# Optimization experiments

Measured on AMD Instinct MI355X. Metric: run time of the kernel, lower is better.

The kernel has to match this reference:

```python
import jax, jax.numpy as jnp
import numpy as np

VOCAB = 10000
EMB = 512
D_IMG = 2048
RNN = 1024
SEQ_LEN = 16
START_TOKEN = VOCAB + 1  # 10001
V_OUT = VOCAB + 3        # 10003


def setup_inputs() -> dict:
    key = jax.random.key(0)
    ks = jax.random.split(key, 24)
    g = lambda k, shape, fan_in: jax.random.normal(k, shape, jnp.float32) / np.sqrt(fan_in)
    inp = {
        "img_features": jax.random.normal(ks[0], (64, 196, D_IMG), jnp.float32),
        "captions": jax.random.randint(ks[1], (64, SEQ_LEN), 0, VOCAB),
        # embedding table
        "emb": g(ks[2], (V_OUT, EMB), EMB),
        # LSTMCell (PyTorch gate order i,f,g,o), stored as [in, 4H]
        "Wih": g(ks[3], (EMB + D_IMG, 4 * RNN), EMB + D_IMG),
        "Whh": g(ks[4], (RNN, 4 * RNN), RNN),
        "bih": jnp.zeros((4 * RNN,), jnp.float32),
        "bhh": jnp.zeros((4 * RNN,), jnp.float32),
        # init_h / init_c
        "Wh0": g(ks[5], (D_IMG, RNN), D_IMG), "bh0": jnp.zeros((RNN,), jnp.float32),
        "Wc0": g(ks[6], (D_IMG, RNN), D_IMG), "bc0": jnp.zeros((RNN,), jnp.float32),
        # f_beta gate
        "Wfb": g(ks[7], (RNN, D_IMG), RNN), "bfb": jnp.zeros((D_IMG,), jnp.float32),
        # deep_output
        "Wout": g(ks[8], (RNN, V_OUT), RNN), "bout": jnp.zeros((V_OUT,), jnp.float32),
        # attention: U (rnn->rnn), W (img->rnn), v (rnn->1)
        "WU": g(ks[9], (RNN, RNN), RNN), "bU": jnp.zeros((RNN,), jnp.float32),
        "WW": g(ks[10], (D_IMG, RNN), D_IMG), "bW": jnp.zeros((RNN,), jnp.float32),
        "Wv": g(ks[11], (RNN, 1), RNN), "bv": jnp.zeros((1,), jnp.float32),
    }
    return inp


def reference(img_features, captions, emb, Wih, Whh, bih, bhh, Wh0, bh0, Wc0, bc0,
              Wfb, bfb, Wout, bout, WU, bU, WW, bW, Wv, bv):
    B = img_features.shape[0]
    # get_target: prepend START token -> [B, T+1]
    start = jnp.full((B, 1), START_TOKEN, dtype=captions.dtype)
    target = jnp.concatenate([start, captions], axis=1)
    embedding = emb[target]                      # [B, T+1, EMB]
    emb_seq = jnp.transpose(embedding, (1, 0, 2))  # [T+1, B, EMB]

    # init LSTM state from mean image features
    avg = img_features.mean(axis=1)              # [B, D_IMG]
    h0 = jnp.tanh(avg @ Wh0 + bh0)
    c0 = jnp.tanh(avg @ Wc0 + bc0)

    # image-side attention projection is timestep-independent
    W_s = img_features @ WW + bW                 # [B, L, RNN]
    b_gates = bih + bhh

    def step(carry, emb_t):
        h, c = carry
        # additive attention
        U_h = h @ WU + bU                        # [B, RNN]
        att = jnp.tanh(W_s + U_h[:, None, :])    # [B, L, RNN]
        e = (att @ Wv).squeeze(-1) + bv          # [B, L]
        alpha = jax.nn.softmax(e, axis=1)
        context = jnp.einsum('bld,bl->bd', img_features, alpha)  # [B, D_IMG]
        gate = jax.nn.sigmoid(h @ Wfb + bfb)
        x = jnp.concatenate([emb_t, gate * context], axis=1)     # [B, EMB+D_IMG]
        # LSTMCell, PyTorch gate order i,f,g,o
        gates = x @ Wih + h @ Whh + b_gates      # [B, 4*RNN]
        i, f, gg, o = jnp.split(gates, 4, axis=1)
        c_new = jax.nn.sigmoid(f) * c + jax.nn.sigmoid(i) * jnp.tanh(gg)
        h_new = jax.nn.sigmoid(o) * jnp.tanh(c_new)
        out = h_new @ Wout + bout                # [B, V_OUT] (dropout=identity, eval mode)
        return (h_new, c_new), (out, alpha)

    (_, _), (preds_t, alphas_t) = jax.lax.scan(step, (h0, c0), emb_seq)
    preds = jnp.transpose(preds_t, (1, 0, 2))    # [B, T+1, V_OUT]
    alphas = jnp.transpose(alphas_t, (1, 0, 2))  # [B, T+1, L]
    return preds, alphas
```

## Files before the change

kernel.cpp:

```cpp
#include <hip/hip_runtime.h>
#include <cstdint>

#define NB    64
#define LIMG  196
#define DIMG  2048
#define RNND  1024
#define EMBD  512
#define TSTEPS 17
#define VOUTD 10003

typedef short bf16x8 __attribute__((ext_vector_type(8)));
typedef float f32x4  __attribute__((ext_vector_type(4)));

__device__ __forceinline__ float fast_sig(float x) {
    return 1.f / (1.f + __expf(-x));
}
__device__ __forceinline__ float fast_tanh(float x) {
    float ax = fabsf(x);
    float e  = __expf(2.f * ax);
    float r  = 1.f - 2.f / (e + 1.f);
    return copysignf(r, x);
}
__device__ __forceinline__ void split_bf(float x, short& hi, short& lo) {
    unsigned u  = __float_as_uint(x);
    unsigned hb = u & 0xffff0000u;
    hi = (short)(u >> 16);
    float r = x - __uint_as_float(hb);
    lo = (short)(__float_as_uint(r) >> 16);
}

__global__ __launch_bounds__(256) void tsplit(
    const float* __restrict__ S1, int ld1,
    const float* __restrict__ S2, int ld2,
    short* __restrict__ outh, short* __restrict__ outl,
    int N, int K, int ksplit, int nsplit)
{
    __shared__ float T[64][65];
    const int k0 = blockIdx.x * 64, n0 = blockIdx.y * 64;
    const int tid = threadIdx.x;
    const int rr = tid >> 2;
    const int cc = (tid & 3) * 16;
    const int kk = k0 + rr;
    const int nn = n0 + cc;
    const float* rp; int col;
    if (nsplit > 0) {
        if (nn >= nsplit) { rp = S2 + (size_t)kk * ld2; col = nn - nsplit; }
        else              { rp = S1 + (size_t)kk * ld1; col = nn; }
    } else {
        if (kk < ksplit)  { rp = S1 + (size_t)kk * ld1; col = nn; }
        else              { rp = S2 + (size_t)(kk - ksplit) * ld2; col = nn; }
    }
#pragma unroll
    for (int j = 0; j < 16; j++)
        T[rr][cc + j] = (nn + j < N) ? rp[col + j] : 0.f;
    __syncthreads();
    const int wn = tid >> 2;
    const int wk = (tid & 3) * 16;
    const int gn = n0 + wn;
    if (gn >= N) return;
    bf16x8 h0, h1, l0, l1;
#pragma unroll
    for (int j = 0; j < 8; j++) {
        short hh, ll;
        split_bf(T[wk + j][wn], hh, ll);     h0[j] = hh; l0[j] = ll;
        split_bf(T[wk + 8 + j][wn], hh, ll); h1[j] = hh; l1[j] = ll;
    }
    const size_t o = (size_t)gn * K + k0 + wk;
    *(bf16x8*)&outh[o]     = h0;
    *(bf16x8*)&outh[o + 8] = h1;
    *(bf16x8*)&outl[o]     = l0;
    *(bf16x8*)&outl[o + 8] = l1;
}

__global__ __launch_bounds__(256) void gemm_bb(
    const float* __restrict__ Af,
    const short* __restrict__ Ah16, const short* __restrict__ Al16,
    const short* __restrict__ Bh16, const short* __restrict__ Bl16,
    const float* __restrict__ bias, float* __restrict__ C,
    int M, int N, int K, int lda, int ldb, int ldc, int pmap,
    int nx, int ny, int gax)
{
    __shared__ short Ah[128 * 40], Al[128 * 40];
    __shared__ short Bh[128 * 40], Bl[128 * 40];

    const int p    = blockIdx.x;
    const int xcd  = p & 7;
    const int slot = p >> 3;
    const int G = gax ? ny : nx;
    const int O = gax ? nx : ny;
    const int qb = G >> 3, qr = G & 7;
    const int cnt = qb + (xcd < qr ? 1 : 0);
    if (slot >= cnt * O) return;
    const int start = xcd * qb + min(xcd, qr);
    const int g = start + slot / O;
    const int o = slot - (slot / O) * O;
    const int n0 = (gax ? o : g) * 128;
    const int m0 = (gax ? g : o) * 128;

    const int tid = threadIdx.x;
    const int lane = tid & 63;
    const int w    = tid >> 6;
    const int wm   = (w >> 1) * 64;
    const int wn   = (w & 1) * 64;
    const int lm   = lane & 15;
    const int lk   = lane >> 4;

    const int ar = tid >> 1;
    const int ac = (tid & 1) * 16;

    f32x4 acc[4][4];
#pragma unroll
    for (int i = 0; i < 4; i++)
#pragma unroll
        for (int j = 0; j < 4; j++) acc[i][j] = (f32x4)0.f;

    for (int k0 = 0; k0 < K; k0 += 32) {
        bf16x8 ah0, ah1, al0, al1;
        if (Af) {
            float f[16];
            if (m0 + ar < M) {
                const float* ap = Af + (size_t)(m0 + ar) * lda + (k0 + ac);
                float4 q0 = *(const float4*)(ap);
                float4 q1 = *(const float4*)(ap + 4);
                float4 q2 = *(const float4*)(ap + 8);
                float4 q3 = *(const float4*)(ap + 12);
                f[0]=q0.x; f[1]=q0.y; f[2]=q0.z; f[3]=q0.w;
                f[4]=q1.x; f[5]=q1.y; f[6]=q1.z; f[7]=q1.w;
                f[8]=q2.x; f[9]=q2.y; f[10]=q2.z; f[11]=q2.w;
                f[12]=q3.x; f[13]=q3.y; f[14]=q3.z; f[15]=q3.w;
            } else {
#pragma unroll
                for (int j = 0; j < 16; j++) f[j] = 0.f;
            }
#pragma unroll
            for (int j = 0; j < 8; j++) {
                short hh, ll;
                split_bf(f[j], hh, ll);     ah0[j] = hh; al0[j] = ll;
                split_bf(f[8 + j], hh, ll); ah1[j] = hh; al1[j] = ll;
            }
        } else {
            const short* pa = Ah16 + (size_t)(m0 + ar) * lda + (k0 + ac);
            ah0 = *(const bf16x8*)pa; ah1 = *(const bf16x8*)(pa + 8);
            const short* qa = Al16 + (size_t)(m0 + ar) * lda + (k0 + ac);
            al0 = *(const bf16x8*)qa; al1 = *(const bf16x8*)(qa + 8);
        }
        const short* pb = Bh16 + (size_t)(n0 + ar) * ldb + (k0 + ac);
        bf16x8 bh0 = *(const bf16x8*)pb, bh1 = *(const bf16x8*)(pb + 8);
        const short* qb2 = Bl16 + (size_t)(n0 + ar) * ldb + (k0 + ac);
        bf16x8 bl0 = *(const bf16x8*)qb2, bl1 = *(const bf16x8*)(qb2 + 8);

        __syncthreads();
        *(bf16x8*)&Ah[ar * 40 + ac]     = ah0;
        *(bf16x8*)&Ah[ar * 40 + ac + 8] = ah1;
        *(bf16x8*)&Al[ar * 40 + ac]     = al0;
        *(bf16x8*)&Al[ar * 40 + ac + 8] = al1;
        *(bf16x8*)&Bh[ar * 40 + ac]     = bh0;
        *(bf16x8*)&Bh[ar * 40 + ac + 8] = bh1;
        *(bf16x8*)&Bl[ar * 40 + ac]     = bl0;
        *(bf16x8*)&Bl[ar * 40 + ac + 8] = bl1;
        __syncthreads();

        bf16x8 afh[4], afl[4], bfh[4], bfl[4];
#pragma unroll
        for (int fm = 0; fm < 4; fm++) {
            const int idx = (wm + fm * 16 + lm) * 40 + lk * 8;
            afh[fm] = *(bf16x8*)&Ah[idx];
            afl[fm] = *(bf16x8*)&Al[idx];
        }
#pragma unroll
        for (int fn = 0; fn < 4; fn++) {
            const int idx = (wn + fn * 16 + lm) * 40 + lk * 8;
            bfh[fn] = *(bf16x8*)&Bh[idx];
            bfl[fn] = *(bf16x8*)&Bl[idx];
        }
#pragma unroll
        for (int fm = 0; fm < 4; fm++)
#pragma unroll
            for (int fn = 0; fn < 4; fn++) {
                acc[fm][fn] = __builtin_amdgcn_mfma_f32_16x16x32_bf16(afh[fm], bfh[fn], acc[fm][fn], 0, 0, 0);
                acc[fm][fn] = __builtin_amdgcn_mfma_f32_16x16x32_bf16(afh[fm], bfl[fn], acc[fm][fn], 0, 0, 0);
                acc[fm][fn] = __builtin_amdgcn_mfma_f32_16x16x32_bf16(afl[fm], bfh[fn], acc[fm][fn], 0, 0, 0);
            }
    }

#pragma unroll
    for (int fm = 0; fm < 4; fm++) {
#pragma unroll
        for (int fn = 0; fn < 4; fn++) {
            const int col = n0 + wn + fn * 16 + lm;
            if (col >= N) continue;
            const float bb = bias ? bias[col] : 0.f;
#pragma unroll
            for (int r = 0; r < 4; r++) {
                const int row = m0 + wm + fm * 16 + lk * 4 + r;
                if (row >= M) continue;
                const size_t orow = pmap ? (size_t)((row & 63) * TSTEPS + (row >> 6))
                                         : (size_t)row;
                C[orow * ldc + col] = acc[fm][fn][r] + bb;
            }
        }
    }
}

__global__ __launch_bounds__(256) void gemm_sk(
    const float* __restrict__ A,
    const short* __restrict__ Bh16, const short* __restrict__ Bl16,
    float* __restrict__ P, int N, int K, int lda, int ldb, int Kc)
{
    __shared__ short Ah[64 * 40], Al[64 * 40];
    __shared__ short Bh[128 * 40], Bl[128 * 40];

    const int tid = threadIdx.x;
    const int n0  = blockIdx.x * 128;
    const int s   = blockIdx.z;
    const int kb  = s * Kc;

    const int lane = tid & 63;
    const int w    = tid >> 6;
    const int wn   = w * 32;
    const int lm   = lane & 15;
    const int lk   = lane >> 4;

    const int a_r = tid >> 2;
    const int a_c = (tid & 3) * 8;
    const int b_r = tid >> 1;
    const int b_c = (tid & 1) * 16;

    f32x4 acc[4][2];
#pragma unroll
    for (int i = 0; i < 4; i++)
#pragma unroll
        for (int j = 0; j < 2; j++) acc[i][j] = (f32x4)0.f;

    for (int k0 = kb; k0 < kb + Kc; k0 += 32) {
        const float* ap = A + (size_t)a_r * lda + (k0 + a_c);
        float4 q0 = *(const float4*)(ap);
        float4 q1 = *(const float4*)(ap + 4);
        float f[8] = {q0.x, q0.y, q0.z, q0.w, q1.x, q1.y, q1.z, q1.w};
        bf16x8 ah, al;
#pragma unroll
        for (int j = 0; j < 8; j++) {
            short hh, ll;
            split_bf(f[j], hh, ll); ah[j] = hh; al[j] = ll;
        }
        const short* pb = Bh16 + (size_t)(n0 + b_r) * ldb + (k0 + b_c);
        bf16x8 bh0 = *(const bf16x8*)pb, bh1 = *(const bf16x8*)(pb + 8);
        const short* qb = Bl16 + (size_t)(n0 + b_r) * ldb + (k0 + b_c);
        bf16x8 bl0 = *(const bf16x8*)qb, bl1 = *(const bf16x8*)(qb + 8);

        __syncthreads();
        *(bf16x8*)&Ah[a_r * 40 + a_c] = ah;
        *(bf16x8*)&Al[a_r * 40 + a_c] = al;
        *(bf16x8*)&Bh[b_r * 40 + b_c]     = bh0;
        *(bf16x8*)&Bh[b_r * 40 + b_c + 8] = bh1;
        *(bf16x8*)&Bl[b_r * 40 + b_c]     = bl0;
        *(bf16x8*)&Bl[b_r * 40 + b_c + 8] = bl1;
        __syncthreads();

        bf16x8 afh[4], afl[4], bfh[2], bfl[2];
#pragma unroll
        for (int fm = 0; fm < 4; fm++) {
            const int idx = (fm * 16 + lm) * 40 + lk * 8;
            afh[fm] = *(bf16x8*)&Ah[idx];
            afl[fm] = *(bf16x8*)&Al[idx];
        }
#pragma unroll
        for (int fn = 0; fn < 2; fn++) {
            const int idx = (wn + fn * 16 + lm) * 40 + lk * 8;
            bfh[fn] = *(bf16x8*)&Bh[idx];
            bfl[fn] = *(bf16x8*)&Bl[idx];
        }
#pragma unroll
        for (int fm = 0; fm < 4; fm++)
#pragma unroll
            for (int fn = 0; fn < 2; fn++) {
                acc[fm][fn] = __builtin_amdgcn_mfma_f32_16x16x32_bf16(afh[fm], bfh[fn], acc[fm][fn], 0, 0, 0);
                acc[fm][fn] = __builtin_amdgcn_mfma_f32_16x16x32_bf16(afh[fm], bfl[fn], acc[fm][fn], 0, 0, 0);
                acc[fm][fn] = __builtin_amdgcn_mfma_f32_16x16x32_bf16(afl[fm], bfh[fn], acc[fm][fn], 0, 0, 0);
            }
    }

    float* Ps = P + (size_t)s * 64 * N;
#pragma unroll
    for (int fm = 0; fm < 4; fm++)
#pragma unroll
        for (int fn = 0; fn < 2; fn++) {
            const int col = n0 + wn + fn * 16 + lm;
#pragma unroll
            for (int r = 0; r < 4; r++) {
                const int row = fm * 16 + lk * 4 + r;
                Ps[(size_t)row * N + col] = acc[fm][fn][r];
            }
        }
}

__global__ __launch_bounds__(256) void gemm64(
    const float* __restrict__ A, const float* __restrict__ B,
    const float* __restrict__ bias, float* __restrict__ C,
    int N, int K, int Kc, int ldc, int act, int direct)
{
    __shared__ float As[16][64];
    __shared__ float Bs[16][68];

    const int tid = threadIdx.x;
    const int n0  = blockIdx.x * 64;
    const int m0  = blockIdx.y * 64;
    const int s   = blockIdx.z;
    const int kb  = s * Kc;
    const int ke  = min(K, kb + Kc);

    const int tm = (tid >> 4) << 2;
    const int tn = (tid & 15) << 2;

    float acc[4][4];
#pragma unroll
    for (int i = 0; i < 4; i++)
#pragma unroll
        for (int j = 0; j < 4; j++) acc[i][j] = 0.f;

    const int a_m = tid >> 2;
    const int a_k = (tid & 3) << 2;
    const int b_k = tid >> 4;
    const int b_n = (tid & 15) << 2;
    const bool n4 = ((N & 3) == 0);

    for (int k0 = kb; k0 < ke; k0 += 16) {
        float4 av = *(const float4*)(A + (size_t)(m0 + a_m) * K + (k0 + a_k));
        float4 bv;
        {
            const int nn = n0 + b_n;
            const float* brow = B + (size_t)(k0 + b_k) * N;
            if (n4) {
                bv = (nn < N) ? *(const float4*)(brow + nn) : make_float4(0.f,0.f,0.f,0.f);
            } else {
                bv.x = (nn + 0 < N) ? brow[nn + 0] : 0.f;
                bv.y = (nn + 1 < N) ? brow[nn + 1] : 0.f;
                bv.z = (nn + 2 < N) ? brow[nn + 2] : 0.f;
                bv.w = (nn + 3 < N) ? brow[nn + 3] : 0.f;
            }
        }
        __syncthreads();
        As[a_k + 0][a_m] = av.x;
        As[a_k + 1][a_m] = av.y;
        As[a_k + 2][a_m] = av.z;
        As[a_k + 3][a_m] = av.w;
        *(float4*)&Bs[b_k][b_n] = bv;
        __syncthreads();
#pragma unroll
        for (int k = 0; k < 16; k++) {
            float4 a4 = *(const float4*)&As[k][tm];
            float4 b4 = *(const float4*)&Bs[k][tn];
            acc[0][0] = fmaf(a4.x, b4.x, acc[0][0]);
            acc[0][1] = fmaf(a4.x, b4.y, acc[0][1]);
            acc[0][2] = fmaf(a4.x, b4.z, acc[0][2]);
            acc[0][3] = fmaf(a4.x, b4.w, acc[0][3]);
            acc[1][0] = fmaf(a4.y, b4.x, acc[1][0]);
            acc[1][1] = fmaf(a4.y, b4.y, acc[1][1]);
            acc[1][2] = fmaf(a4.y, b4.z, acc[1][2]);
            acc[1][3] = fmaf(a4.y, b4.w, acc[1][3]);
            acc[2][0] = fmaf(a4.z, b4.x, acc[2][0]);
            acc[2][1] = fmaf(a4.z, b4.y, acc[2][1]);
            acc[2][2] = fmaf(a4.z, b4.z, acc[2][2]);
            acc[2][3] = fmaf(a4.z, b4.w, acc[2][3]);
            acc[3][0] = fmaf(a4.w, b4.x, acc[3][0]);
            acc[3][1] = fmaf(a4.w, b4.y, acc[3][1]);
            acc[3][2] = fmaf(a4.w, b4.z, acc[3][2]);
            acc[3][3] = fmaf(a4.w, b4.w, acc[3][3]);
        }
    }

    if (direct) {
#pragma unroll
        for (int i = 0; i < 4; i++) {
            const int m = m0 + tm + i;
            const size_t row = (size_t)m * ldc;
#pragma unroll
            for (int j = 0; j < 4; j++) {
                const int n = n0 + tn + j;
                if (n < N) {
                    float v = acc[i][j] + (bias ? bias[n] : 0.f);
                    if (act == 1) v = fast_tanh(v);
                    else if (act == 2) v = fast_sig(v);
                    C[row + n] = v;
                }
            }
        }
    } else {
        float* Pp = C + (size_t)s * 64 * N;
#pragma unroll
        for (int i = 0; i < 4; i++) {
#pragma unroll
            for (int j = 0; j < 4; j++) {
                const int n = n0 + tn + j;
                if (n < N) Pp[(size_t)(tm + i) * N + n] = acc[i][j];
            }
        }
    }
}

__global__ __launch_bounds__(256) void gemm_mfma3(
    const float* __restrict__ A, const float* __restrict__ B,
    const float* __restrict__ bias, float* __restrict__ C,
    int M, int N, int K, int lda, int ldb, int ldc, int pmap)
{
    __shared__ short Ah[128 * 40], Al[128 * 40];
    __shared__ short Bh[128 * 40], Bl[128 * 40];

    const int tid = threadIdx.x;
    const int n0  = blockIdx.x * 128;
    const int m0  = blockIdx.y * 128;

    const int lane = tid & 63;
    const int w    = tid >> 6;
    const int wm   = (w >> 1) * 64;
    const int wn   = (w & 1) * 64;
    const int lm   = lane & 15;
    const int lk   = lane >> 4;

    const int ar = tid >> 1;
    const int ac = (tid & 1) * 16;
    const int kb = (tid & 15) * 2;
    const int c8 = (tid >> 4) * 8;

    const bool bvec = ((ldb & 3) == 0) && (n0 + 128 <= N);

    f32x4 acc[4][4];
#pragma unroll
    for (int i = 0; i < 4; i++)
#pragma unroll
        for (int j = 0; j < 4; j++) acc[i][j] = (f32x4)0.f;

    for (int k0 = 0; k0 < K; k0 += 32) {
        float f[16];
        if (m0 + ar < M) {
            const float* ap = A + (size_t)(m0 + ar) * lda + (k0 + ac);
            float4 q0 = *(const float4*)(ap);
            float4 q1 = *(const float4*)(ap + 4);
            float4 q2 = *(const float4*)(ap + 8);
            float4 q3 = *(const float4*)(ap + 12);
            f[0]=q0.x; f[1]=q0.y; f[2]=q0.z; f[3]=q0.w;
            f[4]=q1.x; f[5]=q1.y; f[6]=q1.z; f[7]=q1.w;
            f[8]=q2.x; f[9]=q2.y; f[10]=q2.z; f[11]=q2.w;
            f[12]=q3.x; f[13]=q3.y; f[14]=q3.z; f[15]=q3.w;
        } else {
#pragma unroll
            for (int j = 0; j < 16; j++) f[j] = 0.f;
        }
        bf16x8 h0, h1, l0, l1;
#pragma unroll
        for (int j = 0; j < 8; j++) {
            short hh, ll;
            split_bf(f[j], hh, ll);     h0[j] = hh; l0[j] = ll;
            split_bf(f[8 + j], hh, ll); h1[j] = hh; l1[j] = ll;
        }
        float g0[8], g1[8];
        if (bvec) {
            const float* bp0 = B + (size_t)(k0 + kb) * ldb + (n0 + c8);
            const float* bp1 = bp0 + ldb;
            float4 q0 = *(const float4*)(bp0);
            float4 q1 = *(const float4*)(bp0 + 4);
            float4 q2 = *(const float4*)(bp1);
            float4 q3 = *(const float4*)(bp1 + 4);
            g0[0]=q0.x; g0[1]=q0.y; g0[2]=q0.z; g0[3]=q0.w;
            g0[4]=q1.x; g0[5]=q1.y; g0[6]=q1.z; g0[7]=q1.w;
            g1[0]=q2.x; g1[1]=q2.y; g1[2]=q2.z; g1[3]=q2.w;
            g1[4]=q3.x; g1[5]=q3.y; g1[6]=q3.z; g1[7]=q3.w;
        } else {
            const float* bp0 = B + (size_t)(k0 + kb) * ldb;
            const float* bp1 = bp0 + ldb;
#pragma unroll
            for (int j = 0; j < 8; j++) {
                const int nn = n0 + c8 + j;
                g0[j] = (nn < N) ? bp0[nn] : 0.f;
                g1[j] = (nn < N) ? bp1[nn] : 0.f;
            }
        }
        __syncthreads();
        *(bf16x8*)&Ah[ar * 40 + ac]     = h0;
        *(bf16x8*)&Ah[ar * 40 + ac + 8] = h1;
        *(bf16x8*)&Al[ar * 40 + ac]     = l0;
        *(bf16x8*)&Al[ar * 40 + ac + 8] = l1;
#pragma unroll
        for (int j = 0; j < 8; j++) {
            short ha, la, hb, lb;
            split_bf(g0[j], ha, la);
            split_bf(g1[j], hb, lb);
            const int ci = (c8 + j) * 40 + kb;
            *(int*)&Bh[ci] = (int)((unsigned short)ha | ((unsigned)(unsigned short)hb << 16));
            *(int*)&Bl[ci] = (int)((unsigned short)la | ((unsigned)(unsigned short)lb << 16));
        }
        __syncthreads();

        bf16x8 afh[4], afl[4], bfh[4], bfl[4];
#pragma unroll
        for (int fm = 0; fm < 4; fm++) {
            const int idx = (wm + fm * 16 + lm) * 40 + lk * 8;
            afh[fm] = *(bf16x8*)&Ah[idx];
            afl[fm] = *(bf16x8*)&Al[idx];
        }
#pragma unroll
        for (int fn = 0; fn < 4; fn++) {
            const int idx = (wn + fn * 16 + lm) * 40 + lk * 8;
            bfh[fn] = *(bf16x8*)&Bh[idx];
            bfl[fn] = *(bf16x8*)&Bl[idx];
        }
#pragma unroll
        for (int fm = 0; fm < 4; fm++)
#pragma unroll
            for (int fn = 0; fn < 4; fn++) {
                acc[fm][fn] = __builtin_amdgcn_mfma_f32_16x16x32_bf16(afh[fm], bfh[fn], acc[fm][fn], 0, 0, 0);
                acc[fm][fn] = __builtin_amdgcn_mfma_f32_16x16x32_bf16(afh[fm], bfl[fn], acc[fm][fn], 0, 0, 0);
                acc[fm][fn] = __builtin_amdgcn_mfma_f32_16x16x32_bf16(afl[fm], bfh[fn], acc[fm][fn], 0, 0, 0);
            }
    }

#pragma unroll
    for (int fm = 0; fm < 4; fm++) {
#pragma unroll
        for (int fn = 0; fn < 4; fn++) {
            const int col = n0 + wn + fn * 16 + lm;
            if (col >= N) continue;
            const float bb = bias ? bias[col] : 0.f;
#pragma unroll
            for (int r = 0; r < 4; r++) {
                const int row = m0 + wm + fm * 16 + lk * 4 + r;
                if (row >= M) continue;
                const size_t orow = pmap ? (size_t)((row & 63) * TSTEPS + (row >> 6))
                                         : (size_t)row;
                C[orow * ldc + col] = acc[fm][fn][r] + bb;
            }
        }
    }
}

__global__ __launch_bounds__(256) void reduce_partials(
    const float* __restrict__ P, int S, int N,
    const float* __restrict__ bias, float* __restrict__ C, int ldc, int act)
{
    const int idx = blockIdx.x * 256 + threadIdx.x;
    const int total = 64 * N;
    if (idx >= total) return;
    const int m = idx / N;
    const int n = idx - m * N;
    float v = bias ? bias[n] : 0.f;
    for (int s = 0; s < S; s++) v += P[(size_t)s * total + idx];
    if (act == 1) v = fast_tanh(v);
    else if (act == 2) v = fast_sig(v);
    else if (act == 3 && n >= RNND) v = fast_sig(v);
    C[(size_t)m * ldc + n] = v;
}

__global__ __launch_bounds__(256) void reduce_lstm(
    const float* __restrict__ P, int S, const float* __restrict__ bsum,
    float* __restrict__ hn, float* __restrict__ c,
    short* __restrict__ hbh, short* __restrict__ hbl)
{
    const int idx = blockIdx.x * 256 + threadIdx.x;
    const int b = idx >> 10, r = idx & 1023;
    const float* pb = P + (size_t)b * 4096;
    float gi = bsum[r], gf = bsum[1024 + r], gg = bsum[2048 + r], go = bsum[3072 + r];
    for (int s = 0; s < S; s++) {
        const float* q = pb + (size_t)s * 64 * 4096;
        gi += q[r]; gf += q[1024 + r]; gg += q[2048 + r]; go += q[3072 + r];
    }
    const float ig = fast_sig(gi);
    const float fg = fast_sig(gf);
    const float g2 = fast_tanh(gg);
    const float og = fast_sig(go);
    const float cn = fg * c[idx] + ig * g2;
    const float hv = og * fast_tanh(cn);
    c[idx]  = cn;
    hn[idx] = hv;
    if (hbh) {
        short hi, lo;
        split_bf(hv, hi, lo);
        hbh[idx] = hi;
        hbl[idx] = lo;
    }
}

__global__ __launch_bounds__(256) void mean_img(
    const float* __restrict__ img, float* __restrict__ avg)
{
    const int b = blockIdx.x;
    const int d = blockIdx.y * 256 + threadIdx.x;
    const float* p = img + (size_t)b * LIMG * DIMG + d;
    float s = 0.f;
    for (int l = 0; l < LIMG; l++) s += p[(size_t)l * DIMG];
    avg[(size_t)b * DIMG + d] = s * (1.f / 196.f);
}

__global__ __launch_bounds__(256) void concat_w(
    const float* __restrict__ WU, const float* __restrict__ Wfb,
    float* __restrict__ Wug)
{
    const int idx = blockIdx.x * 256 + threadIdx.x;
    if (idx >= 1024 * 3072) return;
    const int k = idx / 3072;
    const int j = idx - k * 3072;
    Wug[idx] = (j < 1024) ? WU[(size_t)k * 1024 + j] : Wfb[(size_t)k * 2048 + (j - 1024)];
}

__global__ __launch_bounds__(256) void concat_b(
    const float* __restrict__ bU, const float* __restrict__ bfb,
    const float* __restrict__ bih, const float* __restrict__ bhh,
    float* __restrict__ bug, float* __restrict__ bsum)
{
    const int j = blockIdx.x * 256 + threadIdx.x;
    if (j < 3072) bug[j] = (j < 1024) ? bU[j] : bfb[j - 1024];
    if (j < 4096) bsum[j] = bih[j] + bhh[j];
}

__global__ __launch_bounds__(256) void attn_e(
    const float* __restrict__ Ws, const float* __restrict__ ug,
    const float* __restrict__ Wv, const float* __restrict__ bv,
    float* __restrict__ e)
{
    const int wv   = (blockIdx.x << 2) + (threadIdx.x >> 6);
    const int lane = threadIdx.x & 63;
    const int b    = wv / LIMG;
    const float* wrow = Ws + (size_t)wv * RNND;
    const float* urow = ug + (size_t)b * 3072;
    float acc = 0.f;
#pragma unroll
    for (int k = lane * 4; k < RNND; k += 256) {
        float4 wq = *(const float4*)(wrow + k);
        float4 uq = *(const float4*)(urow + k);
        float4 vq = *(const float4*)(Wv + k);
        acc += fast_tanh(wq.x + uq.x) * vq.x + fast_tanh(wq.y + uq.y) * vq.y
             + fast_tanh(wq.z + uq.z) * vq.z + fast_tanh(wq.w + uq.w) * vq.w;
    }
#pragma unroll
    for (int off = 32; off > 0; off >>= 1) acc += __shfl_down(acc, off);
    if (lane == 0) e[wv] = acc + bv[0];
}

__global__ __launch_bounds__(256) void ctx_fuse(
    const float* __restrict__ e, const float* __restrict__ img,
    const float* __restrict__ ug, const float* __restrict__ embt,
    const int* __restrict__ captions, const float* __restrict__ h,
    float* __restrict__ x, float* __restrict__ alphas_out, int t)
{
    __shared__ float al[256];
    __shared__ float red[256];
    const int b = blockIdx.x, y = blockIdx.y, tid = threadIdx.x;

    const float v = (tid < LIMG) ? e[b * LIMG + tid] : -3.0e38f;
    red[tid] = v; __syncthreads();
    for (int s = 128; s > 0; s >>= 1) {
        if (tid < s) red[tid] = fmaxf(red[tid], red[tid + s]);
        __syncthreads();
    }
    const float mx = red[0]; __syncthreads();
    const float ex = (tid < LIMG) ? __expf(v - mx) : 0.f;
    red[tid] = ex; __syncthreads();
    for (int s = 128; s > 0; s >>= 1) {
        if (tid < s) red[tid] += red[tid + s];
        __syncthreads();
    }
    const float inv = 1.f / red[0];
    al[tid] = ex * inv;
    __syncthreads();

    if (y == 0) {
        if (tid < LIMG)
            alphas_out[(size_t)b * (TSTEPS * LIMG) + t * LIMG + tid] = al[tid];
        const int tok = (t == 0) ? 10001 : captions[b * 16 + (t - 1)];
        for (int j = tid; j < EMBD; j += 256)
            x[(size_t)b * 3584 + j] = embt[(size_t)tok * EMBD + j];
        for (int j = tid; j < RNND; j += 256)
            x[(size_t)b * 3584 + 2560 + j] = h[(size_t)b * RNND + j];
    } else {
        const int d0 = (y - 1) * 512 + tid * 2;
        const float* ib = img + (size_t)b * LIMG * DIMG + d0;
        float a0 = 0.f, a1 = 0.f;
#pragma unroll 4
        for (int l = 0; l < LIMG; l++) {
            float2 q = *(const float2*)(ib + (size_t)l * DIMG);
            a0 = fmaf(al[l], q.x, a0);
            a1 = fmaf(al[l], q.y, a1);
        }
        const float g0 = ug[(size_t)b * 3072 + 1024 + d0];
        const float g1 = ug[(size_t)b * 3072 + 1024 + d0 + 1];
        x[(size_t)b * 3584 + EMBD + d0]     = g0 * a0;
        x[(size_t)b * 3584 + EMBD + d0 + 1] = g1 * a1;
    }
}

__global__ __launch_bounds__(256) void softmax_alpha(
    const float* __restrict__ e, float* __restrict__ alpha,
    float* __restrict__ alphas_out, int t)
{
    __shared__ float red[256];
    const int b = blockIdx.x, tid = threadIdx.x;
    const float v = (tid < LIMG) ? e[b * LIMG + tid] : -3.0e38f;
    red[tid] = v; __syncthreads();
    for (int s = 128; s > 0; s >>= 1) {
        if (tid < s) red[tid] = fmaxf(red[tid], red[tid + s]);
        __syncthreads();
    }
    const float mx = red[0]; __syncthreads();
    const float ex = (tid < LIMG) ? __expf(v - mx) : 0.f;
    red[tid] = ex; __syncthreads();
    for (int s = 128; s > 0; s >>= 1) {
        if (tid < s) red[tid] += red[tid + s];
        __syncthreads();
    }
    const float inv = 1.f / red[0];
    if (tid < LIMG) {
        const float a = ex * inv;
        alpha[b * LIMG + tid] = a;
        alphas_out[(size_t)b * (TSTEPS * LIMG) + t * LIMG + tid] = a;
    }
}

__global__ __launch_bounds__(128) void assemble_x(
    const float* __restrict__ img, const float* __restrict__ alpha,
    const float* __restrict__ ug, const float* __restrict__ emb,
    const int* __restrict__ captions, const float* __restrict__ h,
    float* __restrict__ x, int t, int stride)
{
    const int b = blockIdx.x, y = blockIdx.y, tid = threadIdx.x;
    if (y < 4) {
        const int tok = (t == 0) ? 10001 : captions[b * 16 + (t - 1)];
        const int j = y * 128 + tid;
        x[(size_t)b * stride + j] = emb[(size_t)tok * EMBD + j];
    } else if (y < 20) {
        __shared__ float al[LIMG];
        for (int i = tid; i < LIMG; i += 128) al[i] = alpha[b * LIMG + i];
        __syncthreads();
        const int d = (y - 4) * 128 + tid;
        const float* ib = img + (size_t)b * LIMG * DIMG + d;
        float accv = 0.f;
#pragma unroll 4
        for (int l = 0; l < LIMG; l++) accv = fmaf(al[l], ib[(size_t)l * DIMG], accv);
        const float g = ug[(size_t)b * 3072 + 1024 + d];
        x[(size_t)b * stride + EMBD + d] = g * accv;
    } else {
        const int j = (y - 20) * 128 + tid;
        x[(size_t)b * stride + 2560 + j] = h[(size_t)b * RNND + j];
    }
}

extern "C" void kernel_launch(void* const* d_in, const int* in_sizes, int n_in,
                              void* d_out, int out_size, void* d_ws, size_t ws_size,
                              hipStream_t stream)
{
    const float* img      = (const float*)d_in[0];
    const int*   captions = (const int*)d_in[1];
    const float* emb      = (const float*)d_in[2];
    const float* Wih      = (const float*)d_in[3];
    const float* Whh      = (const float*)d_in[4];
    const float* bih      = (const float*)d_in[5];
    const float* bhh      = (const float*)d_in[6];
    const float* Wh0      = (const float*)d_in[7];
    const float* bh0      = (const float*)d_in[8];
    const float* Wc0      = (const float*)d_in[9];
    const float* bc0      = (const float*)d_in[10];
    const float* Wfb      = (const float*)d_in[11];
    const float* bfb      = (const float*)d_in[12];
    const float* Wout     = (const float*)d_in[13];
    const float* bout     = (const float*)d_in[14];
    const float* WU       = (const float*)d_in[15];
    const float* bU       = (const float*)d_in[16];
    const float* WW       = (const float*)d_in[17];
    const float* bW       = (const float*)d_in[18];
    const float* Wv       = (const float*)d_in[19];
    const float* bv       = (const float*)d_in[20];

    float* preds      = (float*)d_out;
    float* alphas_out = preds + (size_t)NB * TSTEPS * VOUTD;

    const size_t NEED = 190000000;

    if (ws_size >= NEED) {
        float* w = (float*)d_ws;
        float* Ws    = w; w += (size_t)12544 * 1024;
        float* ug    = w; w += (size_t)64 * 3072;
        float* P     = w; w += (size_t)8 * 64 * 4096;
        float* e     = w; w += (size_t)64 * LIMG;
        float* alpha = w; w += (size_t)64 * LIMG;
        float* xh    = w; w += (size_t)64 * 3584;
        float* h     = w; w += (size_t)64 * RNND;
        float* c     = w; w += (size_t)64 * RNND;
        float* avg   = w; w += (size_t)64 * DIMG;
        float* bsum  = w; w += 4096;
        float* bug   = w; w += 3072;
        short* u = (short*)w;
        short* Hbh     = u; u += (size_t)1280 * 1024;
        short* Hbl     = u; u += (size_t)1280 * 1024;
        short* WWTh    = u; u += (size_t)1024 * 2048;
        short* WWTl    = u; u += (size_t)1024 * 2048;
        short* WugTh   = u; u += (size_t)3072 * 1024;
        short* WugTl   = u; u += (size_t)3072 * 1024;
        short* WfullTh = u; u += (size_t)4096 * 3584;
        short* WfullTl = u; u += (size_t)4096 * 3584;
        short* WoutTh  = u; u += (size_t)10112 * 1024;
        short* WoutTl  = u; u += (size_t)10112 * 1024;

        mean_img<<<dim3(NB, 8), 256, 0, stream>>>(img, avg);
        gemm64<<<dim3(16, 1, 8), 256, 0, stream>>>(avg, Wh0, nullptr, P, 1024, 2048, 256, 0, 0, 0);
        reduce_partials<<<256, 256, 0, stream>>>(P, 8, 1024, bh0, h, 1024, 1);
        gemm64<<<dim3(16, 1, 8), 256, 0, stream>>>(avg, Wc0, nullptr, P, 1024, 2048, 256, 0, 0, 0);
        reduce_partials<<<256, 256, 0, stream>>>(P, 8, 1024, bc0, c, 1024, 1);
        concat_b<<<16, 256, 0, stream>>>(bU, bfb, bih, bhh, bug, bsum);

        tsplit<<<dim3(32, 16), 256, 0, stream>>>(WW, 1024, WW, 1024, WWTh, WWTl, 1024, 2048, 2048, 0);
        tsplit<<<dim3(16, 48), 256, 0, stream>>>(WU, 1024, Wfb, 2048, WugTh, WugTl, 3072, 1024, 1024, 1024);
        tsplit<<<dim3(56, 64), 256, 0, stream>>>(Wih, 4096, Whh, 4096, WfullTh, WfullTl, 4096, 3584, 2560, 0);
        tsplit<<<dim3(16, 157), 256, 0, stream>>>(Wout, VOUTD, Wout, VOUTD, WoutTh, WoutTl, VOUTD, 1024, 1024, 0);

        gemm_bb<<<832, 256, 0, stream>>>(img, nullptr, nullptr, WWTh, WWTl,
                                         bW, Ws, 12544, 1024, 2048, 2048, 2048, 1024, 0,
                                         8, 98, 1);

        for (int t = 0; t < TSTEPS; t++) {
            gemm_sk<<<dim3(24, 1, 8), 256, 0, stream>>>(h, WugTh, WugTl, P, 3072, 1024, 1024, 1024, 128);
            reduce_partials<<<768, 256, 0, stream>>>(P, 8, 3072, bug, ug, 3072, 3);
            attn_e<<<3136, 256, 0, stream>>>(Ws, ug, Wv, bv, e);
            ctx_fuse<<<dim3(NB, 5), 256, 0, stream>>>(e, img, ug, emb, captions, h, xh, alphas_out, t);
            gemm_sk<<<dim3(32, 1, 7), 256, 0, stream>>>(xh, WfullTh, WfullTl, P, 4096, 3584, 3584, 3584, 512);
            reduce_lstm<<<256, 256, 0, stream>>>(P, 7, bsum, h, c,
                                                 Hbh + (size_t)(t + 1) * 65536,
                                                 Hbl + (size_t)(t + 1) * 65536);
        }

        gemm_bb<<<720, 256, 0, stream>>>(nullptr, Hbh + 65536, Hbl + 65536,
                                         WoutTh, WoutTl, bout, preds,
                                         1088, VOUTD, 1024, 1024, 1024, VOUTD, 1,
                                         79, 9, 0);
    } else {
        float* w = (float*)d_ws;
        float* Ws    = w; w += (size_t)12544 * 1024;
        float* ug    = w; w += (size_t)64 * 3072;
        float* P     = w; w += (size_t)12 * 64 * 4096;
        float* e     = w; w += (size_t)64 * LIMG;
        float* alpha = w; w += (size_t)64 * LIMG;
        float* x     = w; w += (size_t)64 * 2560;
        float* Hh    = w; w += (size_t)18 * 64 * RNND;
        float* c     = w; w += (size_t)64 * RNND;
        float* avg   = w; w += (size_t)64 * DIMG;
        float* bsum  = w; w += 4096;
        float* Wug   = w; w += (size_t)1024 * 3072;
        float* bug   = w; w += 3072;

        mean_img<<<dim3(NB, 8), 256, 0, stream>>>(img, avg);
        gemm64<<<dim3(16, 1, 8), 256, 0, stream>>>(avg, Wh0, nullptr, P, 1024, 2048, 256, 0, 0, 0);
        reduce_partials<<<256, 256, 0, stream>>>(P, 8, 1024, bh0, Hh, 1024, 1);
        gemm64<<<dim3(16, 1, 8), 256, 0, stream>>>(avg, Wc0, nullptr, P, 1024, 2048, 256, 0, 0, 0);
        reduce_partials<<<256, 256, 0, stream>>>(P, 8, 1024, bc0, c, 1024, 1);
        concat_b<<<16, 256, 0, stream>>>(bU, bfb, bih, bhh, bug, bsum);
        concat_w<<<12288, 256, 0, stream>>>(WU, Wfb, Wug);
        gemm_mfma3<<<dim3(8, 98), 256, 0, stream>>>(img, WW, bW, Ws,
                                                    12544, 1024, 2048, 2048, 1024, 1024, 0);
        for (int t = 0; t < TSTEPS; t++) {
            const float* hc = Hh + (size_t)t * 64 * RNND;
            float*       hn = Hh + (size_t)(t + 1) * 64 * RNND;
            gemm64<<<dim3(48, 1, 8), 256, 0, stream>>>(hc, Wug, nullptr, P, 3072, 1024, 128, 0, 0, 0);
            reduce_partials<<<768, 256, 0, stream>>>(P, 8, 3072, bug, ug, 3072, 3);
            attn_e<<<3136, 256, 0, stream>>>(Ws, ug, Wv, bv, e);
            softmax_alpha<<<NB, 256, 0, stream>>>(e, alpha, alphas_out, t);
            assemble_x<<<dim3(NB, 20), 128, 0, stream>>>(img, alpha, ug, emb, captions, hc, x, t, 2560);
            gemm64<<<dim3(64, 1, 8), 256, 0, stream>>>(x, Wih, nullptr, P, 4096, 2560, 320, 0, 0, 0);
            gemm64<<<dim3(64, 1, 4), 256, 0, stream>>>(hc, Whh, nullptr, P + (size_t)8 * 64 * 4096,
                                                       4096, 1024, 256, 0, 0, 0);
            reduce_lstm<<<256, 256, 0, stream>>>(P, 12, bsum, hn, c, nullptr, nullptr);
        }
        gemm_mfma3<<<dim3(79, 9), 256, 0, stream>>>(Hh + (size_t)64 * RNND, Wout, bout, preds,
                                                    TSTEPS * 64, VOUTD, 1024, 1024, VOUTD, VOUTD, 1);
    }
}
```

Before: 1.769 ms.

## Prefetch next K tile into registers and drop split-K for attention projection GEMM

Both bf16-split GEMM kernels now load the next K tile from global memory into registers while the current tile's MFMAs run, overlapping memory latency with compute. Separately, the per-step h @ [WU|Wfb] GEMM no longer uses 8-way split-K. It runs with a single K slice and writes the bias and sigmoid epilogue directly, which removes one reduce_partials launch per timestep. In exchange the recurrent GEMM now has only 24 blocks, each looping over the full K=1024, which leaves most CUs idle, and the prefetch registers raise register pressure.

Result: slower. 2.097 ms (+18.5%).

```diff
diff --git a/kernel.cpp b/kernel.cpp
--- a/kernel.cpp
+++ b/kernel.cpp
@@ -114,8 +114,9 @@
 #pragma unroll
         for (int j = 0; j < 4; j++) acc[i][j] = (f32x4)0.f;
 
-    for (int k0 = 0; k0 < K; k0 += 32) {
-        bf16x8 ah0, ah1, al0, al1;
+    bf16x8 rah0, rah1, ral0, ral1, rbh0, rbh1, rbl0, rbl1;
+
+    auto load_tile = [&](int k0) {
         if (Af) {
             float f[16];
             if (m0 + ar < M) {
@@ -135,30 +136,34 @@
 #pragma unroll
             for (int j = 0; j < 8; j++) {
                 short hh, ll;
-                split_bf(f[j], hh, ll);     ah0[j] = hh; al0[j] = ll;
-                split_bf(f[8 + j], hh, ll); ah1[j] = hh; al1[j] = ll;
+                split_bf(f[j], hh, ll);     rah0[j] = hh; ral0[j] = ll;
+                split_bf(f[8 + j], hh, ll); rah1[j] = hh; ral1[j] = ll;
             }
         } else {
             const short* pa = Ah16 + (size_t)(m0 + ar) * lda + (k0 + ac);
-            ah0 = *(const bf16x8*)pa; ah1 = *(const bf16x8*)(pa + 8);
+            rah0 = *(const bf16x8*)pa; rah1 = *(const bf16x8*)(pa + 8);
             const short* qa = Al16 + (size_t)(m0 + ar) * lda + (k0 + ac);
-            al0 = *(const bf16x8*)qa; al1 = *(const bf16x8*)(qa + 8);
+            ral0 = *(const bf16x8*)qa; ral1 = *(const bf16x8*)(qa + 8);
         }
         const short* pb = Bh16 + (size_t)(n0 + ar) * ldb + (k0 + ac);
-        bf16x8 bh0 = *(const bf16x8*)pb, bh1 = *(const bf16x8*)(pb + 8);
+        rbh0 = *(const bf16x8*)pb; rbh1 = *(const bf16x8*)(pb + 8);
         const short* qb2 = Bl16 + (size_t)(n0 + ar) * ldb + (k0 + ac);
-        bf16x8 bl0 = *(const bf16x8*)qb2, bl1 = *(const bf16x8*)(qb2 + 8);
-
-        __syncthreads();
-        *(bf16x8*)&Ah[ar * 40 + ac]     = ah0;
-        *(bf16x8*)&Ah[ar * 40 + ac + 8] = ah1;
-        *(bf16x8*)&Al[ar * 40 + ac]     = al0;
-        *(bf16x8*)&Al[ar * 40 + ac + 8] = al1;
-        *(bf16x8*)&Bh[ar * 40 + ac]     = bh0;
-        *(bf16x8*)&Bh[ar * 40 + ac + 8] = bh1;
-        *(bf16x8*)&Bl[ar * 40 + ac]     = bl0;
-        *(bf16x8*)&Bl[ar * 40 + ac + 8] = bl1;
-        __syncthreads();
+        rbl0 = *(const bf16x8*)qb2; rbl1 = *(const bf16x8*)(qb2 + 8);
+    };
+
+    load_tile(0);
+    for (int k0 = 0; k0 < K; k0 += 32) {
+        __syncthreads();
+        *(bf16x8*)&Ah[ar * 40 + ac]     = rah0;
+        *(bf16x8*)&Ah[ar * 40 + ac + 8] = rah1;
+        *(bf16x8*)&Al[ar * 40 + ac]     = ral0;
+        *(bf16x8*)&Al[ar * 40 + ac + 8] = ral1;
+        *(bf16x8*)&Bh[ar * 40 + ac]     = rbh0;
+        *(bf16x8*)&Bh[ar * 40 + ac + 8] = rbh1;
+        *(bf16x8*)&Bl[ar * 40 + ac]     = rbl0;
+        *(bf16x8*)&Bl[ar * 40 + ac + 8] = rbl1;
+        __syncthreads();
+        if (k0 + 32 < K) load_tile(k0 + 32);
 
         bf16x8 afh[4], afl[4], bfh[4], bfl[4];
 #pragma unroll
@@ -205,7 +210,8 @@
 __global__ __launch_bounds__(256) void gemm_sk(
     const float* __restrict__ A,
     const short* __restrict__ Bh16, const short* __restrict__ Bl16,
-    float* __restrict__ P, int N, int K, int lda, int ldb, int Kc)
+    float* __restrict__ C, const float* __restrict__ bias,
+    int N, int K, int lda, int ldb, int Kc, int ldc, int act)
 {
     __shared__ short Ah[64 * 40], Al[64 * 40];
     __shared__ short Bh[128 * 40], Bl[128 * 40];
@@ -232,30 +238,34 @@
 #pragma unroll
         for (int j = 0; j < 2; j++) acc[i][j] = (f32x4)0.f;
 
-    for (int k0 = kb; k0 < kb + Kc; k0 += 32) {
+    bf16x8 rah, ral, rbh0, rbh1, rbl0, rbl1;
+    auto load_tile = [&](int k0) {
         const float* ap = A + (size_t)a_r * lda + (k0 + a_c);
         float4 q0 = *(const float4*)(ap);
         float4 q1 = *(const float4*)(ap + 4);
         float f[8] = {q0.x, q0.y, q0.z, q0.w, q1.x, q1.y, q1.z, q1.w};
-        bf16x8 ah, al;
 #pragma unroll
         for (int j = 0; j < 8; j++) {
             short hh, ll;
-            split_bf(f[j], hh, ll); ah[j] = hh; al[j] = ll;
+            split_bf(f[j], hh, ll); rah[j] = hh; ral[j] = ll;
         }
         const short* pb = Bh16 + (size_t)(n0 + b_r) * ldb + (k0 + b_c);
-        bf16x8 bh0 = *(const bf16x8*)pb, bh1 = *(const bf16x8*)(pb + 8);
+        rbh0 = *(const bf16x8*)pb; rbh1 = *(const bf16x8*)(pb + 8);
         const short* qb = Bl16 + (size_t)(n0 + b_r) * ldb + (k0 + b_c);
-        bf16x8 bl0 = *(const bf16x8*)qb, bl1 = *(const bf16x8*)(qb + 8);
-
-        __syncthreads();
-        *(bf16x8*)&Ah[a_r * 40 + a_c] = ah;
-        *(bf16x8*)&Al[a_r * 40 + a_c] = al;
-        *(bf16x8*)&Bh[b_r * 40 + b_c]     = bh0;
-        *(bf16x8*)&Bh[b_r * 40 + b_c + 8] = bh1;
-        *(bf16x8*)&Bl[b_r * 40 + b_c]     = bl0;
-        *(bf16x8*)&Bl[b_r * 40 + b_c + 8] = bl1;
-        __syncthreads();
+        rbl0 = *(const bf16x8*)qb; rbl1 = *(const bf16x8*)(qb + 8);
+    };
+
+    load_tile(kb);
+    for (int k0 = kb; k0 < kb + Kc; k0 += 32) {
+        __syncthreads();
+        *(bf16x8*)&Ah[a_r * 40 + a_c] = rah;
+        *(bf16x8*)&Al[a_r * 40 + a_c] = ral;
+        *(bf16x8*)&Bh[b_r * 40 + b_c]     = rbh0;
+        *(bf16x8*)&Bh[b_r * 40 + b_c + 8] = rbh1;
+        *(bf16x8*)&Bl[b_r * 40 + b_c]     = rbl0;
+        *(bf16x8*)&Bl[b_r * 40 + b_c + 8] = rbl1;
+        __syncthreads();
+        if (k0 + 32 < kb + Kc) load_tile(k0 + 32);
 
         bf16x8 afh[4], afl[4], bfh[2], bfl[2];
 #pragma unroll
@@ -280,18 +290,35 @@
             }
     }
 
-    float* Ps = P + (size_t)s * 64 * N;
-#pragma unroll
-    for (int fm = 0; fm < 4; fm++)
-#pragma unroll
-        for (int fn = 0; fn < 2; fn++) {
-            const int col = n0 + wn + fn * 16 + lm;
-#pragma unroll
-            for (int r = 0; r < 4; r++) {
-                const int row = fm * 16 + lk * 4 + r;
-                Ps[(size_t)row * N + col] = acc[fm][fn][r];
-            }
-        }
+    if (Kc == K) {
+#pragma unroll
+        for (int fm = 0; fm < 4; fm++)
+#pragma unroll
+            for (int fn = 0; fn < 2; fn++) {
+                const int col = n0 + wn + fn * 16 + lm;
+                const float bb = bias ? bias[col] : 0.f;
+#pragma unroll
+                for (int r = 0; r < 4; r++) {
+                    const int row = fm * 16 + lk * 4 + r;
+                    float v = acc[fm][fn][r] + bb;
+                    if (act == 3 && col >= RNND) v = fast_sig(v);
+                    C[(size_t)row * ldc + col] = v;
+                }
+            }
+    } else {
+        float* Ps = C + (size_t)s * 64 * N;
+#pragma unroll
+        for (int fm = 0; fm < 4; fm++)
+#pragma unroll
+            for (int fn = 0; fn < 2; fn++) {
+                const int col = n0 + wn + fn * 16 + lm;
+#pragma unroll
+                for (int r = 0; r < 4; r++) {
+                    const int row = fm * 16 + lk * 4 + r;
+                    Ps[(size_t)row * N + col] = acc[fm][fn][r];
+                }
+            }
+    }
 }
 
 __global__ __launch_bounds__(256) void gemm64(
@@ -815,11 +842,12 @@
                                          8, 98, 1);
 
         for (int t = 0; t < TSTEPS; t++) {
-            gemm_sk<<<dim3(24, 1, 8), 256, 0, stream>>>(h, WugTh, WugTl, P, 3072, 1024, 1024, 1024, 128);
-            reduce_partials<<<768, 256, 0, stream>>>(P, 8, 3072, bug, ug, 3072, 3);
+            gemm_sk<<<dim3(24, 1, 1), 256, 0, stream>>>(h, WugTh, WugTl, ug, bug,
+                                                        3072, 1024, 1024, 1024, 1024, 3072, 3);
             attn_e<<<3136, 256, 0, stream>>>(Ws, ug, Wv, bv, e);
             ctx_fuse<<<dim3(NB, 5), 256, 0, stream>>>(e, img, ug, emb, captions, h, xh, alphas_out, t);
-            gemm_sk<<<dim3(32, 1, 7), 256, 0, stream>>>(xh, WfullTh, WfullTl, P, 4096, 3584, 3584, 3584, 512);
+            gemm_sk<<<dim3(32, 1, 7), 256, 0, stream>>>(xh, WfullTh, WfullTl, P, nullptr,
+                                                        4096, 3584, 3584, 3584, 512, 0, 0);
             reduce_lstm<<<256, 256, 0, stream>>>(P, 7, bsum, h, c,
                                                  Hbh + (size_t)(t + 1) * 65536,
                                                  Hbl + (size_t)(t + 1) * 65536);
```

## Replace XCD-swizzled 128x128 GEMM with 64x128 tiles and register prefetch

Applied to the files above, without the earlier changes.

Replaces the 128x128-tile GEMM, which mapped blocks to XCDs with a swizzle, with a 64x128-tile GEMM on a plain 2D grid. The new kernel prefetches the next K-tile into registers while the current one is computed. Dropping the M bounds checks relies on M being a multiple of 64. Smaller tiles give more blocks but less operand reuse, and the XCD-aware L2 locality of the old mapping is lost.

New measurement: 1.891 ms (median of 2 runs). 6.9% more time.

```diff
diff --git a/kernel.cpp b/kernel.cpp
--- a/kernel.cpp
+++ b/kernel.cpp
@@ -72,103 +72,80 @@
     *(bf16x8*)&outl[o + 8] = l1;
 }
 
-__global__ __launch_bounds__(256) void gemm_bb(
+__global__ __launch_bounds__(256) void gemm_mt(
     const float* __restrict__ Af,
     const short* __restrict__ Ah16, const short* __restrict__ Al16,
     const short* __restrict__ Bh16, const short* __restrict__ Bl16,
     const float* __restrict__ bias, float* __restrict__ C,
-    int M, int N, int K, int lda, int ldb, int ldc, int pmap,
-    int nx, int ny, int gax)
-{
-    __shared__ short Ah[128 * 40], Al[128 * 40];
+    int N, int K, int lda, int ldb, int ldc, int pmap)
+{
+    __shared__ short Ah[64 * 40], Al[64 * 40];
     __shared__ short Bh[128 * 40], Bl[128 * 40];
 
-    const int p    = blockIdx.x;
-    const int xcd  = p & 7;
-    const int slot = p >> 3;
-    const int G = gax ? ny : nx;
-    const int O = gax ? nx : ny;
-    const int qb = G >> 3, qr = G & 7;
-    const int cnt = qb + (xcd < qr ? 1 : 0);
-    if (slot >= cnt * O) return;
-    const int start = xcd * qb + min(xcd, qr);
-    const int g = start + slot / O;
-    const int o = slot - (slot / O) * O;
-    const int n0 = (gax ? o : g) * 128;
-    const int m0 = (gax ? g : o) * 128;
-
     const int tid = threadIdx.x;
+    const int n0  = blockIdx.x * 128;
+    const int m0  = blockIdx.y * 64;
+
     const int lane = tid & 63;
     const int w    = tid >> 6;
-    const int wm   = (w >> 1) * 64;
-    const int wn   = (w & 1) * 64;
+    const int wn   = w * 32;
     const int lm   = lane & 15;
     const int lk   = lane >> 4;
 
-    const int ar = tid >> 1;
-    const int ac = (tid & 1) * 16;
-
-    f32x4 acc[4][4];
+    const int a_r = tid >> 2;
+    const int a_c = (tid & 3) * 8;
+    const int b_r = tid >> 1;
+    const int b_c = (tid & 1) * 16;
+
+    f32x4 acc[4][2];
 #pragma unroll
     for (int i = 0; i < 4; i++)
 #pragma unroll
-        for (int j = 0; j < 4; j++) acc[i][j] = (f32x4)0.f;
-
-    for (int k0 = 0; k0 < K; k0 += 32) {
-        bf16x8 ah0, ah1, al0, al1;
+        for (int j = 0; j < 2; j++) acc[i][j] = (f32x4)0.f;
+
+    bf16x8 rah, ral, rbh0, rbh1, rbl0, rbl1;
+    auto load_tile = [&](int k0) {
         if (Af) {
-            float f[16];
-            if (m0 + ar < M) {
-                const float* ap = Af + (size_t)(m0 + ar) * lda + (k0 + ac);
-                float4 q0 = *(const float4*)(ap);
-                float4 q1 = *(const float4*)(ap + 4);
-                float4 q2 = *(const float4*)(ap + 8);
-                float4 q3 = *(const float4*)(ap + 12);
-                f[0]=q0.x; f[1]=q0.y; f[2]=q0.z; f[3]=q0.w;
-                f[4]=q1.x; f[5]=q1.y; f[6]=q1.z; f[7]=q1.w;
-                f[8]=q2.x; f[9]=q2.y; f[10]=q2.z; f[11]=q2.w;
-                f[12]=q3.x; f[13]=q3.y; f[14]=q3.z; f[15]=q3.w;
-            } else {
-#pragma unroll
-                for (int j = 0; j < 16; j++) f[j] = 0.f;
-            }
+            const float* ap = Af + (size_t)(m0 + a_r) * lda + (k0 + a_c);
+            float4 q0 = *(const float4*)(ap);
+            float4 q1 = *(const float4*)(ap + 4);
+            float f[8] = {q0.x, q0.y, q0.z, q0.w, q1.x, q1.y, q1.z, q1.w};
 #pragma unroll
             for (int j = 0; j < 8; j++) {
                 short hh, ll;
-                split_bf(f[j], hh, ll);     ah0[j] = hh; al0[j] = ll;
-                split_bf(f[8 + j], hh, ll); ah1[j] = hh; al1[j] = ll;
+                split_bf(f[j], hh, ll); rah[j] = hh; ral[j] = ll;
             }
         } else {
-            const short* pa = Ah16 + (size_t)(m0 + ar) * lda + (k0 + ac);
-            ah0 = *(const bf16x8*)pa; ah1 = *(const bf16x8*)(pa + 8);
-            const short* qa = Al16 + (size_t)(m0 + ar) * lda + (k0 + ac);
-            al0 = *(const bf16x8*)qa; al1 = *(const bf16x8*)(qa + 8);
-        }
-        const short* pb = Bh16 + (size_t)(n0 + ar) * ldb + (k0 + ac);
-        bf16x8 bh0 = *(const bf16x8*)pb, bh1 = *(const bf16x8*)(pb + 8);
-        const short* qb2 = Bl16 + (size_t)(n0 + ar) * ldb + (k0 + ac);
-        bf16x8 bl0 = *(const bf16x8*)qb2, bl1 = *(const bf16x8*)(qb2 + 8);
-
-        __syncthreads();
-        *(bf16x8*)&Ah[ar * 40 + ac]     = ah0;
-        *(bf16x8*)&Ah[ar * 40 + ac + 8] = ah1;
-        *(bf16x8*)&Al[ar * 40 + ac]     = al0;
-        *(bf16x8*)&Al[ar * 40 + ac + 8] = al1;
-        *(bf16x8*)&Bh[ar * 40 + ac]     = bh0;
-        *(bf16x8*)&Bh[ar * 40 + ac + 8] = bh1;
-        *(bf16x8*)&Bl[ar * 40 + ac]     = bl0;
-        *(bf16x8*)&Bl[ar * 40 + ac + 8] = bl1;
-        __syncthreads();
-
-        bf16x8 afh[4], afl[4], bfh[4], bfl[4];
+            rah = *(const bf16x8*)(Ah16 + (size_t)(m0 + a_r) * lda + (k0 + a_c));
+            ral = *(const bf16x8*)(Al16 + (size_t)(m0 + a_r) * lda + (k0 + a_c));
+        }
+        const short* pb = Bh16 + (size_t)(n0 + b_r) * ldb + (k0 + b_c);
+        rbh0 = *(const bf16x8*)pb; rbh1 = *(const bf16x8*)(pb + 8);
+        const short* qb = Bl16 + (size_t)(n0 + b_r) * ldb + (k0 + b_c);
+        rbl0 = *(const bf16x8*)qb; rbl1 = *(const bf16x8*)(qb + 8);
+    };
+
+    load_tile(0);
+    for (int k0 = 0; k0 < K; k0 += 32) {
+        __syncthreads();
+        *(bf16x8*)&Ah[a_r * 40 + a_c] = rah;
+        *(bf16x8*)&Al[a_r * 40 + a_c] = ral;
+        *(bf16x8*)&Bh[b_r * 40 + b_c]     = rbh0;
+        *(bf16x8*)&Bh[b_r * 40 + b_c + 8] = rbh1;
+        *(bf16x8*)&Bl[b_r * 40 + b_c]     = rbl0;
+        *(bf16x8*)&Bl[b_r * 40 + b_c + 8] = rbl1;
+        __syncthreads();
+        if (k0 + 32 < K) load_tile(k0 + 32);
+
+        bf16x8 afh[4], afl[4], bfh[2], bfl[2];
 #pragma unroll
         for (int fm = 0; fm < 4; fm++) {
-            const int idx = (wm + fm * 16 + lm) * 40 + lk * 8;
+            const int idx = (fm * 16 + lm) * 40 + lk * 8;
             afh[fm] = *(bf16x8*)&Ah[idx];
             afl[fm] = *(bf16x8*)&Al[idx];
         }
 #pragma unroll
-        for (int fn = 0; fn < 4; fn++) {
+        for (int fn = 0; fn < 2; fn++) {
             const int idx = (wn + fn * 16 + lm) * 40 + lk * 8;
             bfh[fn] = *(bf16x8*)&Bh[idx];
             bfl[fn] = *(bf16x8*)&Bl[idx];
@@ -176,7 +153,7 @@
 #pragma unroll
         for (int fm = 0; fm < 4; fm++)
 #pragma unroll
-            for (int fn = 0; fn < 4; fn++) {
+            for (int fn = 0; fn < 2; fn++) {
                 acc[fm][fn] = __builtin_amdgcn_mfma_f32_16x16x32_bf16(afh[fm], bfh[fn], acc[fm][fn], 0, 0, 0);
                 acc[fm][fn] = __builtin_amdgcn_mfma_f32_16x16x32_bf16(afh[fm], bfl[fn], acc[fm][fn], 0, 0, 0);
                 acc[fm][fn] = __builtin_amdgcn_mfma_f32_16x16x32_bf16(afl[fm], bfh[fn], acc[fm][fn], 0, 0, 0);
@@ -184,22 +161,20 @@
     }
 
 #pragma unroll
-    for (int fm = 0; fm < 4; fm++) {
-#pragma unroll
-        for (int fn = 0; fn < 4; fn++) {
+    for (int fm = 0; fm < 4; fm++)
+#pragma unroll
+        for (int fn = 0; fn < 2; fn++) {
             const int col = n0 + wn + fn * 16 + lm;
             if (col >= N) continue;
             const float bb = bias ? bias[col] : 0.f;
 #pragma unroll
             for (int r = 0; r < 4; r++) {
-                const int row = m0 + wm + fm * 16 + lk * 4 + r;
-                if (row >= M) continue;
+                const int row = m0 + fm * 16 + lk * 4 + r;
                 const size_t orow = pmap ? (size_t)((row & 63) * TSTEPS + (row >> 6))
                                          : (size_t)row;
                 C[orow * ldc + col] = acc[fm][fn][r] + bb;
             }
         }
-    }
 }
 
 __global__ __launch_bounds__(256) void gemm_sk(
@@ -810,9 +785,8 @@
         tsplit<<<dim3(56, 64), 256, 0, stream>>>(Wih, 4096, Whh, 4096, WfullTh, WfullTl, 4096, 3584, 2560, 0);
         tsplit<<<dim3(16, 157), 256, 0, stream>>>(Wout, VOUTD, Wout, VOUTD, WoutTh, WoutTl, VOUTD, 1024, 1024, 0);
 
-        gemm_bb<<<832, 256, 0, stream>>>(img, nullptr, nullptr, WWTh, WWTl,
-                                         bW, Ws, 12544, 1024, 2048, 2048, 2048, 1024, 0,
-                                         8, 98, 1);
+        gemm_mt<<<dim3(8, 196), 256, 0, stream>>>(img, nullptr, nullptr, WWTh, WWTl,
+                                                  bW, Ws, 1024, 2048, 2048, 2048, 1024, 0);
 
         for (int t = 0; t < TSTEPS; t++) {
             gemm_sk<<<dim3(24, 1, 8), 256, 0, stream>>>(h, WugTh, WugTl, P, 3072, 1024, 1024, 1024, 128);
@@ -825,10 +799,9 @@
                                                  Hbl + (size_t)(t + 1) * 65536);
         }
 
-        gemm_bb<<<720, 256, 0, stream>>>(nullptr, Hbh + 65536, Hbl + 65536,
-                                         WoutTh, WoutTl, bout, preds,
-                                         1088, VOUTD, 1024, 1024, 1024, VOUTD, 1,
-                                         79, 9, 0);
+        gemm_mt<<<dim3(79, 17), 256, 0, stream>>>(nullptr, Hbh + 65536, Hbl + 65536,
+                                                  WoutTh, WoutTl, bout, preds,
+                                                  VOUTD, 1024, 1024, 1024, VOUTD, 1);
     } else {
         float* w = (float*)d_ws;
         float* Ws    = w; w += (size_t)12544 * 1024;
```
